# Kernel optimization log

Measured on AMD Instinct MI355X. Metric: run time of the kernel, lower is better.

The kernel has to match this reference:

```python
import jax, jax.numpy as jnp
import numpy as np

EPS = 1e-5

def _round_ste(x):
    # straight-through round (identical value in fwd; STE grad in bwd module)
    return x + jax.lax.stop_gradient(jnp.round(x) - x)

def _quant_weight(w, bits):
    # per-tensor symmetric absmax quantization to `bits` bits (BitNet-style)
    qb = float(2 ** (bits - 1) - 1)
    scale = qb / jnp.maximum(jnp.max(jnp.abs(w)), EPS)
    return _round_ste(jnp.clip(w * scale, -qb, qb)) / scale

def _quant_act(x):
    # per-token 8-bit absmax activation quantization
    qb = 127.0
    scale = qb / jnp.maximum(jnp.max(jnp.abs(x), axis=-1, keepdims=True), EPS)
    return _round_ste(jnp.clip(x * scale, -qb, qb)) / scale

def _layernorm(x, gamma, beta):
    mu = jnp.mean(x, axis=-1, keepdims=True)
    var = jnp.mean(jnp.square(x - mu), axis=-1, keepdims=True)
    return (x - mu) * jax.lax.rsqrt(var + EPS) * gamma + beta

def _qlinear(x, w, b, bits):
    return jnp.einsum('btd,fd->btf', _quant_act(x), _quant_weight(w, bits)) + b

def setup_inputs() -> dict:
    key = jax.random.key(0)
    ks = jax.random.split(key, 4)
    B, T, D, F = 8, 2048, 1024, 4096
    return {
        'x': jax.random.normal(ks[0], (B, T, D), dtype=jnp.float32),
        'mask': jnp.ones((B, T, 1), dtype=jnp.float32),
        'ln_gamma': jnp.ones((D,), dtype=jnp.float32),
        'ln_beta': jnp.zeros((D,), dtype=jnp.float32),
        'w1': jax.random.normal(ks[1], (F, D), dtype=jnp.float32) * (1.0 / np.sqrt(D)),
        'b1': jnp.zeros((F,), dtype=jnp.float32),
        'w2': jax.random.normal(ks[2], (D, F), dtype=jnp.float32) * (1.0 / np.sqrt(F)),
        'b2': jnp.zeros((D,), dtype=jnp.float32),
        'bitwidth': 8,
    }

def reference(x, mask, ln_gamma, ln_beta, w1, b1, w2, b2, bitwidth):
    y = _layernorm(x, ln_gamma, ln_beta)           # [B,T,D]
    y = _qlinear(y, w1, b1, bitwidth)              # [B,T,F]
    y = y * jax.nn.sigmoid(y)                      # swish
    y = _qlinear(y, w2, b2, bitwidth)              # [B,T,D]
    seq_mask = mask[:, :, 0][..., None]            # [B,T,1]
    y = y * seq_mask
    return x + 0.5 * y
```

## Files before the change

kernel.cpp:

```cpp
#include <hip/hip_runtime.h>
#include <hip/hip_bf16.h>
#include <stdint.h>


typedef int v4i __attribute__((ext_vector_type(4)));
typedef int v16i __attribute__((ext_vector_type(16)));

#define BK 128

__device__ __forceinline__ float wave_max64(float v) {
#pragma unroll
  for (int off = 32; off; off >>= 1) v = fmaxf(v, __shfl_xor(v, off, 64));
  return v;
}

__device__ __forceinline__ void load16_to_lds(const int8_t* g, int8_t* l) {
  __builtin_amdgcn_global_load_lds((const __attribute__((address_space(1))) void*)g,
                                   (__attribute__((address_space(3))) void*)l, 16, 0, 0);
}

__global__ __launch_bounds__(256) void absmax_kernel(const float* __restrict__ w, int n4,
                                                     int* __restrict__ slot) {
  float m = 0.f;
  const float4* w4 = (const float4*)w;
  for (int i = blockIdx.x * 256 + threadIdx.x; i < n4; i += gridDim.x * 256) {
    float4 v = w4[i];
    m = fmaxf(fmaxf(fabsf(v.x), fabsf(v.y)), fmaxf(fmaxf(fabsf(v.z), fabsf(v.w)), m));
  }
  m = wave_max64(m);
  __shared__ float sm[4];
  int lane = threadIdx.x & 63, wv = threadIdx.x >> 6;
  if (!lane) sm[wv] = m;
  __syncthreads();
  if (!threadIdx.x) {
    m = fmaxf(fmaxf(sm[0], sm[1]), fmaxf(sm[2], sm[3]));
    atomicMax(slot, __float_as_int(m));
  }
}

__global__ void scales_kernel(const int* __restrict__ wmax, const int* __restrict__ bits,
                              float* __restrict__ scal) {
  float qb = (float)((1 << (bits[0] - 1)) - 1);
  scal[2] = qb / fmaxf(__int_as_float(wmax[0]), 1e-5f);
  scal[3] = qb / fmaxf(__int_as_float(wmax[1]), 1e-5f);
  scal[4] = qb;
}

__global__ __launch_bounds__(256) void wquant_kernel(const float* __restrict__ w,
                                                     const float* __restrict__ scal, int which,
                                                     int8_t* __restrict__ out) {
  float s = scal[2 + which], qb = scal[4];
  int i = blockIdx.x * 256 + threadIdx.x;
  float4 v = ((const float4*)w)[i];
  char4 q;
  q.x = (char)(int)rintf(fminf(fmaxf(v.x * s, -qb), qb));
  q.y = (char)(int)rintf(fminf(fmaxf(v.y * s, -qb), qb));
  q.z = (char)(int)rintf(fminf(fmaxf(v.z * s, -qb), qb));
  q.w = (char)(int)rintf(fminf(fmaxf(v.w * s, -qb), qb));
  ((char4*)out)[i] = q;
}

__global__ __launch_bounds__(256) void ln_quant_kernel(const float* __restrict__ x,
                                                       const float* __restrict__ gamma,
                                                       const float* __restrict__ beta,
                                                       int8_t* __restrict__ xq,
                                                       float* __restrict__ xscale) {
  const int wv = threadIdx.x >> 6;
  const int lane = threadIdx.x & 63;
  const int row = blockIdx.x * 4 + wv;
  const float4* xr = (const float4*)(x + (size_t)row * 1024);
  float4 v[4];
#pragma unroll
  for (int k = 0; k < 4; ++k) v[k] = xr[lane + k * 64];
  float s = 0.f, ss = 0.f;
#pragma unroll
  for (int k = 0; k < 4; ++k) {
    s += v[k].x + v[k].y + v[k].z + v[k].w;
    ss = fmaf(v[k].x, v[k].x, fmaf(v[k].y, v[k].y, fmaf(v[k].z, v[k].z, fmaf(v[k].w, v[k].w, ss))));
  }
#pragma unroll
  for (int off = 32; off; off >>= 1) {
    s += __shfl_xor(s, off, 64);
    ss += __shfl_xor(ss, off, 64);
  }
  const float mu = s * (1.f / 1024.f);
  const float var = ss * (1.f / 1024.f) - mu * mu;
  const float rstd = rsqrtf(var + 1e-5f);
  const float4* g4 = (const float4*)gamma;
  const float4* b4 = (const float4*)beta;
  float am = 0.f;
#pragma unroll
  for (int k = 0; k < 4; ++k) {
    const float4 g = g4[lane + k * 64];
    const float4 b = b4[lane + k * 64];
    v[k].x = (v[k].x - mu) * rstd * g.x + b.x;
    v[k].y = (v[k].y - mu) * rstd * g.y + b.y;
    v[k].z = (v[k].z - mu) * rstd * g.z + b.z;
    v[k].w = (v[k].w - mu) * rstd * g.w + b.w;
    am = fmaxf(am, fmaxf(fmaxf(fabsf(v[k].x), fabsf(v[k].y)), fmaxf(fabsf(v[k].z), fabsf(v[k].w))));
  }
  am = wave_max64(am);
  const float scale = 127.f / fmaxf(am, 1e-5f);
  char4* qr = (char4*)(xq + (size_t)row * 1024);
#pragma unroll
  for (int k = 0; k < 4; ++k) {
    char4 q;
    q.x = (char)(int)rintf(fminf(fmaxf(v[k].x * scale, -127.f), 127.f));
    q.y = (char)(int)rintf(fminf(fmaxf(v[k].y * scale, -127.f), 127.f));
    q.z = (char)(int)rintf(fminf(fmaxf(v[k].z * scale, -127.f), 127.f));
    q.w = (char)(int)rintf(fminf(fmaxf(v[k].w * scale, -127.f), 127.f));
    qr[lane + k * 64] = q;
  }
  if (!lane) xscale[row] = scale;
}

__global__ __launch_bounds__(256) void hquant_kernel(const ushort* __restrict__ h,
                                                     int8_t* __restrict__ hq,
                                                     float* __restrict__ hscale) {
  const int wv = threadIdx.x >> 6;
  const int lane = threadIdx.x & 63;
  const int row = blockIdx.x * 4 + wv;
  const int4* p = (const int4*)(h + (size_t)row * 4096);
  float f[64];
#pragma unroll
  for (int k = 0; k < 8; ++k) {
    union { int4 i4; ushort u[8]; } ua;
    ua.i4 = p[lane + k * 64];
#pragma unroll
    for (int i = 0; i < 8; ++i) f[k * 8 + i] = __uint_as_float((unsigned)ua.u[i] << 16);
  }
  float am = 0.f;
#pragma unroll
  for (int i = 0; i < 64; ++i) am = fmaxf(am, fabsf(f[i]));
  am = wave_max64(am);
  const float scale = 127.f / fmaxf(am, 1e-5f);
  int2* qr = (int2*)(hq + (size_t)row * 4096);
#pragma unroll
  for (int k = 0; k < 8; ++k) {
    union { int2 i2; char c[8]; } q;
#pragma unroll
    for (int i = 0; i < 8; ++i)
      q.c[i] = (char)(int)rintf(fminf(fmaxf(f[k * 8 + i] * scale, -127.f), 127.f));
    qr[lane + k * 64] = q.i2;
  }
  if (!lane) hscale[row] = scale;
}

template <int K, int BMt, int BNt>
__device__ __forceinline__ void gemm_core(const int8_t* __restrict__ A,
                                          const int8_t* __restrict__ B, int8_t* As, int8_t* Bs,
                                          v16i (&acc)[BMt / 64][BNt / 64]) {
  constexpr int AM = BMt / 64, AN = BNt / 64;
  const int tid = threadIdx.x;
  const int lane = tid & 63;
  const int wave = tid >> 6;
  const int wm = (wave & 1) * (BMt / 2);
  const int wn = (wave >> 1) * (BNt / 2);
  const int lrow = lane & 31;
  const int half = lane >> 5;
  const int x7 = lrow & 7;
  const size_t m0 = (size_t)blockIdx.y * BMt;
  const size_t n0 = (size_t)blockIdx.x * BNt;

  const int r = tid >> 3;
  const int cs = ((tid & 7) ^ (r & 7)) << 4;
  const int8_t* ga = A + (m0 + r) * K + cs;
  const int8_t* gb = B + (n0 + r) * K + cs;
  int8_t* la = As + tid * 16;
  int8_t* lb = Bs + tid * 16;

  for (int k0 = 0; k0 < K; k0 += BK) {
    __syncthreads();
#pragma unroll
    for (int t = 0; t < BMt / 32; ++t)
      load16_to_lds(ga + (size_t)(t * 32) * K + k0, la + t * 4096);
#pragma unroll
    for (int t = 0; t < BNt / 32; ++t)
      load16_to_lds(gb + (size_t)(t * 32) * K + k0, lb + t * 4096);
    __syncthreads();
#pragma unroll
    for (int ks = 0; ks < 4; ++ks) {
      const int so = ((ks * 2 + half) ^ x7) << 4;
      v4i af[AM], bf[AN];
#pragma unroll
      for (int i = 0; i < AM; ++i)
        af[i] = *(const v4i*)(As + (wm + i * 32 + lrow) * 128 + so);
#pragma unroll
      for (int j = 0; j < AN; ++j)
        bf[j] = *(const v4i*)(Bs + (wn + j * 32 + lrow) * 128 + so);
#pragma unroll
      for (int i = 0; i < AM; ++i)
#pragma unroll
        for (int j = 0; j < AN; ++j)
          acc[i][j] = __builtin_amdgcn_mfma_i32_32x32x32_i8(af[i], bf[j], acc[i][j], 0, 0, 0);
    }
  }
}

__global__ __launch_bounds__(256, 2) void gemm1_kernel(const int8_t* __restrict__ Aq,
                                                       const int8_t* __restrict__ Bq,
                                                       const float* __restrict__ xscale,
                                                       const float* __restrict__ scal,
                                                       const float* __restrict__ bias,
                                                       ushort* __restrict__ H) {
  __shared__ __align__(16) int8_t As[128 * 128];
  __shared__ __align__(16) int8_t Bs[256 * 128];
  v16i acc[2][4] = {};
  gemm_core<1024, 128, 256>(Aq, Bq, As, Bs, acc);
  const float sw1 = scal[2];
  const int lane = threadIdx.x & 63;
  const int wave = threadIdx.x >> 6;
  const int m0 = blockIdx.y * 128 + (wave & 1) * 64;
  const int n0 = blockIdx.x * 256 + (wave >> 1) * 128;
  const int cn = lane & 31;
  const int h4 = (lane >> 5) << 2;
#pragma unroll
  for (int i = 0; i < 2; ++i) {
#pragma unroll
    for (int reg = 0; reg < 16; ++reg) {
      const int row = (reg & 3) + ((reg >> 2) << 3) + h4;
      const int m = m0 + i * 32 + row;
      const float rcp = 1.0f / (xscale[m] * sw1);
#pragma unroll
      for (int j = 0; j < 4; ++j) {
        const int n = n0 + j * 32 + cn;
        const float v = (float)acc[i][j][reg] * rcp + bias[n];
        const float hsw = v / (1.0f + __expf(-v));
        __hip_bfloat16 hb = __float2bfloat16(hsw);
        H[(size_t)m * 4096 + n] = *(const ushort*)&hb;
      }
    }
  }
}

__global__ __launch_bounds__(256, 2) void gemm2_kernel(const int8_t* __restrict__ Aq,
                                                       const int8_t* __restrict__ Bq,
                                                       const float* __restrict__ hscale,
                                                       const float* __restrict__ scal,
                                                       const float* __restrict__ bias,
                                                       const float* __restrict__ x,
                                                       const float* __restrict__ mask,
                                                       float* __restrict__ out) {
  __shared__ __align__(16) int8_t As[256 * 128];
  __shared__ __align__(16) int8_t Bs[128 * 128];
  v16i acc[4][2] = {};
  gemm_core<4096, 256, 128>(Aq, Bq, As, Bs, acc);
  const float sw2 = scal[3];
  const int lane = threadIdx.x & 63;
  const int wave = threadIdx.x >> 6;
  const int m0 = blockIdx.y * 256 + (wave & 1) * 128;
  const int n0 = blockIdx.x * 128 + (wave >> 1) * 64;
  const int cn = lane & 31;
  const int h4 = (lane >> 5) << 2;
#pragma unroll
  for (int i = 0; i < 4; ++i) {
#pragma unroll
    for (int reg = 0; reg < 16; ++reg) {
      const int row = (reg & 3) + ((reg >> 2) << 3) + h4;
      const int m = m0 + i * 32 + row;
      const float rcp = 1.0f / (hscale[m] * sw2);
      const float mk = 0.5f * mask[m];
#pragma unroll
      for (int j = 0; j < 2; ++j) {
        const int n = n0 + j * 32 + cn;
        const float v = (float)acc[i][j][reg] * rcp + bias[n];
        const size_t idx = (size_t)m * 1024 + n;
        out[idx] = x[idx] + mk * v;
      }
    }
  }
}

extern "C" void kernel_launch(void* const* d_in, const int* in_sizes, int n_in, void* d_out,
                              int out_size, void* d_ws, size_t ws_size, hipStream_t stream) {
  const float* x = (const float*)d_in[0];
  const float* mask = (const float*)d_in[1];
  const float* gamma = (const float*)d_in[2];
  const float* beta = (const float*)d_in[3];
  const float* w1 = (const float*)d_in[4];
  const float* b1 = (const float*)d_in[5];
  const float* w2 = (const float*)d_in[6];
  const float* b2 = (const float*)d_in[7];
  const int* bits = (const int*)d_in[8];
  float* out = (float*)d_out;

  char* ws = (char*)d_ws;
  int* wmax = (int*)ws;
  float* scal = (float*)ws;
  float* xscale = (float*)(ws + (1u << 20));
  float* hscale = (float*)(ws + (2u << 20));
  int8_t* w1q = (int8_t*)(ws + (4u << 20));
  int8_t* w2q = (int8_t*)(ws + (8u << 20));
  int8_t* xq = (int8_t*)(ws + (12u << 20));
  int8_t* hq = (int8_t*)(ws + (28u << 20));
  ushort* h = (ushort*)(ws + (size_t)(92u << 20));

  const int NW = 4096 * 1024;

  absmax_kernel<<<1024, 256, 0, stream>>>(w1, NW / 4, wmax + 0);
  absmax_kernel<<<1024, 256, 0, stream>>>(w2, NW / 4, wmax + 1);
  scales_kernel<<<1, 1, 0, stream>>>(wmax, bits, scal);
  wquant_kernel<<<NW / 1024, 256, 0, stream>>>(w1, scal, 0, w1q);
  wquant_kernel<<<NW / 1024, 256, 0, stream>>>(w2, scal, 1, w2q);
  ln_quant_kernel<<<4096, 256, 0, stream>>>(x, gamma, beta, xq, xscale);
  gemm1_kernel<<<dim3(4096 / 256, 16384 / 128), 256, 0, stream>>>(xq, w1q, xscale, scal, b1, h);
  hquant_kernel<<<4096, 256, 0, stream>>>(h, hq, hscale);
  gemm2_kernel<<<dim3(1024 / 128, 16384 / 256), 256, 0, stream>>>(hq, w2q, hscale, scal, b2, x,
                                                                  mask, out);
}
```

Before: 431.7 us.

## Load GEMM B operand directly from global into registers, bypassing LDS

The shared GEMM core now stages only the A tile in LDS. Each wave reads its B (weight) fragments straight from global memory into registers in MFMA operand layout, which removes the B LDS buffer and its LDS read traffic. GEMM2 is retiled from 256x128 to 128x256 so both GEMMs use the same core. In exchange, B fragments are no longer shared between the two waves that need the same columns, so global/L2 traffic for B doubles. The direct loads are 16-byte strided row reads with no prefetch, so their latency is exposed before each barrier.

Measured after the change: 567.6 us. 31.5% more time.

```diff
diff --git a/kernel.cpp b/kernel.cpp
--- a/kernel.cpp
+++ b/kernel.cpp
@@ -146,53 +146,51 @@
   if (!lane) hscale[row] = scale;
 }
 
-template <int K, int BMt, int BNt>
-__device__ __forceinline__ void gemm_core(const int8_t* __restrict__ A,
-                                          const int8_t* __restrict__ B, int8_t* As, int8_t* Bs,
-                                          v16i (&acc)[BMt / 64][BNt / 64]) {
-  constexpr int AM = BMt / 64, AN = BNt / 64;
+template <int K>
+__device__ __forceinline__ void gemm_core_bd(const int8_t* __restrict__ A,
+                                             const int8_t* __restrict__ B, int8_t* As,
+                                             v16i (&acc)[2][4]) {
   const int tid = threadIdx.x;
   const int lane = tid & 63;
   const int wave = tid >> 6;
-  const int wm = (wave & 1) * (BMt / 2);
-  const int wn = (wave >> 1) * (BNt / 2);
+  const int wm = (wave & 1) * 64;
+  const int wn = (wave >> 1) * 128;
   const int lrow = lane & 31;
   const int half = lane >> 5;
   const int x7 = lrow & 7;
-  const size_t m0 = (size_t)blockIdx.y * BMt;
-  const size_t n0 = (size_t)blockIdx.x * BNt;
+  const size_t m0 = (size_t)blockIdx.y * 128;
+  const size_t n0 = (size_t)blockIdx.x * 256;
 
   const int r = tid >> 3;
   const int cs = ((tid & 7) ^ (r & 7)) << 4;
   const int8_t* ga = A + (m0 + r) * K + cs;
-  const int8_t* gb = B + (n0 + r) * K + cs;
   int8_t* la = As + tid * 16;
-  int8_t* lb = Bs + tid * 16;
+  const int8_t* gb = B + (size_t)(n0 + wn + lrow) * K + half * 16;
 
   for (int k0 = 0; k0 < K; k0 += BK) {
     __syncthreads();
 #pragma unroll
-    for (int t = 0; t < BMt / 32; ++t)
+    for (int t = 0; t < 4; ++t)
       load16_to_lds(ga + (size_t)(t * 32) * K + k0, la + t * 4096);
-#pragma unroll
-    for (int t = 0; t < BNt / 32; ++t)
-      load16_to_lds(gb + (size_t)(t * 32) * K + k0, lb + t * 4096);
+    v4i bf[4][4];
+#pragma unroll
+    for (int ks = 0; ks < 4; ++ks)
+#pragma unroll
+      for (int j = 0; j < 4; ++j)
+        bf[ks][j] = *(const v4i*)(gb + (size_t)(j * 32) * K + k0 + ks * 32);
     __syncthreads();
 #pragma unroll
     for (int ks = 0; ks < 4; ++ks) {
       const int so = ((ks * 2 + half) ^ x7) << 4;
-      v4i af[AM], bf[AN];
-#pragma unroll
-      for (int i = 0; i < AM; ++i)
+      v4i af[2];
+#pragma unroll
+      for (int i = 0; i < 2; ++i)
         af[i] = *(const v4i*)(As + (wm + i * 32 + lrow) * 128 + so);
 #pragma unroll
-      for (int j = 0; j < AN; ++j)
-        bf[j] = *(const v4i*)(Bs + (wn + j * 32 + lrow) * 128 + so);
-#pragma unroll
-      for (int i = 0; i < AM; ++i)
-#pragma unroll
-        for (int j = 0; j < AN; ++j)
-          acc[i][j] = __builtin_amdgcn_mfma_i32_32x32x32_i8(af[i], bf[j], acc[i][j], 0, 0, 0);
+      for (int i = 0; i < 2; ++i)
+#pragma unroll
+        for (int j = 0; j < 4; ++j)
+          acc[i][j] = __builtin_amdgcn_mfma_i32_32x32x32_i8(af[i], bf[ks][j], acc[i][j], 0, 0, 0);
     }
   }
 }
@@ -204,9 +202,8 @@
                                                        const float* __restrict__ bias,
                                                        ushort* __restrict__ H) {
   __shared__ __align__(16) int8_t As[128 * 128];
-  __shared__ __align__(16) int8_t Bs[256 * 128];
   v16i acc[2][4] = {};
-  gemm_core<1024, 128, 256>(Aq, Bq, As, Bs, acc);
+  gemm_core_bd<1024>(Aq, Bq, As, acc);
   const float sw1 = scal[2];
   const int lane = threadIdx.x & 63;
   const int wave = threadIdx.x >> 6;
@@ -241,19 +238,18 @@
                                                        const float* __restrict__ x,
                                                        const float* __restrict__ mask,
                                                        float* __restrict__ out) {
-  __shared__ __align__(16) int8_t As[256 * 128];
-  __shared__ __align__(16) int8_t Bs[128 * 128];
-  v16i acc[4][2] = {};
-  gemm_core<4096, 256, 128>(Aq, Bq, As, Bs, acc);
+  __shared__ __align__(16) int8_t As[128 * 128];
+  v16i acc[2][4] = {};
+  gemm_core_bd<4096>(Aq, Bq, As, acc);
   const float sw2 = scal[3];
   const int lane = threadIdx.x & 63;
   const int wave = threadIdx.x >> 6;
-  const int m0 = blockIdx.y * 256 + (wave & 1) * 128;
-  const int n0 = blockIdx.x * 128 + (wave >> 1) * 64;
+  const int m0 = blockIdx.y * 128 + (wave & 1) * 64;
+  const int n0 = blockIdx.x * 256 + (wave >> 1) * 128;
   const int cn = lane & 31;
   const int h4 = (lane >> 5) << 2;
 #pragma unroll
-  for (int i = 0; i < 4; ++i) {
+  for (int i = 0; i < 2; ++i) {
 #pragma unroll
     for (int reg = 0; reg < 16; ++reg) {
       const int row = (reg & 3) + ((reg >> 2) << 3) + h4;
@@ -261,7 +257,7 @@
       const float rcp = 1.0f / (hscale[m] * sw2);
       const float mk = 0.5f * mask[m];
 #pragma unroll
-      for (int j = 0; j < 2; ++j) {
+      for (int j = 0; j < 4; ++j) {
         const int n = n0 + j * 32 + cn;
         const float v = (float)acc[i][j][reg] * rcp + bias[n];
         const size_t idx = (size_t)m * 1024 + n;
@@ -305,6 +301,6 @@
   ln_quant_kernel<<<4096, 256, 0, stream>>>(x, gamma, beta, xq, xscale);
   gemm1_kernel<<<dim3(4096 / 256, 16384 / 128), 256, 0, stream>>>(xq, w1q, xscale, scal, b1, h);
   hquant_kernel<<<4096, 256, 0, stream>>>(h, hq, hscale);
-  gemm2_kernel<<<dim3(1024 / 128, 16384 / 256), 256, 0, stream>>>(hq, w2q, hscale, scal, b2, x,
+  gemm2_kernel<<<dim3(1024 / 256, 16384 / 128), 256, 0, stream>>>(hq, w2q, hscale, scal, b2, x,
                                                                   mask, out);
 }
```
